# Kernel optimization log

Hardware: AMD Instinct MI355X
Metric: run time of the kernel (lower is better)

Reference implementation:

```python
import jax, jax.numpy as jnp
import numpy as np

B, N, K, C, D_IN, D_OUT = 64, 207, 32, 8, 64, 64


def setup_inputs() -> dict:
    key = jax.random.key(0)
    k1, k2, k3 = jax.random.split(key, 3)
    clustered_index_topk = jax.random.randint(k1, (B, N, K), 0, C)
    weightedDinput_topk = jax.random.normal(k2, (B, N, K, D_IN), dtype=jnp.float32)
    W = jax.random.normal(k3, (C, D_OUT, D_IN), dtype=jnp.float32) * 0.05
    return {"clustered_index_topk": clustered_index_topk,
            "weightedDinput_topk": weightedDinput_topk,
            "W": W}


def reference(clustered_index_topk, weightedDinput_topk, W):
    # one-hot over classes: [B, N, K, C]
    onehot = (clustered_index_topk[..., None] == jnp.arange(C)).astype(weightedDinput_topk.dtype)
    # per-class masked sum over top-k neighbors: [B, N, C, D_IN]
    sums = jnp.einsum('bnkc,bnkd->bncd', onehot, weightedDinput_topk)
    # per-class counts, clamped to >= 1 (matches torch.clamp(class_count, 1))
    counts = jnp.maximum(onehot.sum(axis=2), 1.0)  # [B, N, C]
    mean = sums / counts[..., None]
    # per-class Linear (weight [out, in], no bias) + Tanh -> [B, N, C, D_OUT]
    out = jnp.tanh(jnp.einsum('bncd,cod->bnco', mean, W))
    return out
```

## Files before the change

### kernel.cpp

```cpp
#include <hip/hip_runtime.h>
#include <cstddef>

#define BB 64
#define NN 207
#define KK 32
#define CC 8
#define DIN 64
#define DOUT 64
#define TILE 16
#define NT 13
#define MPADH 68

__device__ __forceinline__ float fast_tanh(float v) {
    float e = __expf(2.0f * v);
    return 1.0f - 2.0f * __builtin_amdgcn_rcpf(e + 1.0f);
}

__device__ __forceinline__ unsigned int f2bf(float f) {
    union { float f; unsigned int u; } v; v.f = f;
    return (v.u + 0x7fffu + ((v.u >> 16) & 1u)) >> 16;
}

__device__ __forceinline__ void fma16(float4& a, const float4 m,
                                      const float4 w0, const float4 w1,
                                      const float4 w2, const float4 w3) {
    a.x = fmaf(m.x, w0.x, a.x); a.y = fmaf(m.x, w0.y, a.y);
    a.z = fmaf(m.x, w0.z, a.z); a.w = fmaf(m.x, w0.w, a.w);
    a.x = fmaf(m.y, w1.x, a.x); a.y = fmaf(m.y, w1.y, a.y);
    a.z = fmaf(m.y, w1.z, a.z); a.w = fmaf(m.y, w1.w, a.w);
    a.x = fmaf(m.z, w2.x, a.x); a.y = fmaf(m.z, w2.y, a.y);
    a.z = fmaf(m.z, w2.z, a.z); a.w = fmaf(m.z, w2.w, a.w);
    a.x = fmaf(m.w, w3.x, a.x); a.y = fmaf(m.w, w3.y, a.y);
    a.z = fmaf(m.w, w3.z, a.z); a.w = fmaf(m.w, w3.w, a.w);
}

template<bool USE_WT>
__device__ __forceinline__ void load_w4(const float* __restrict__ Wtc,
                                        const float* __restrict__ Wc,
                                        int o0, int dc,
                                        float4& w0, float4& w1, float4& w2, float4& w3) {
    if (USE_WT) {
        w0 = *(const float4*)(Wtc + (size_t)(dc * 4 + 0) * DOUT);
        w1 = *(const float4*)(Wtc + (size_t)(dc * 4 + 1) * DOUT);
        w2 = *(const float4*)(Wtc + (size_t)(dc * 4 + 2) * DOUT);
        w3 = *(const float4*)(Wtc + (size_t)(dc * 4 + 3) * DOUT);
    } else {
        float4 a0 = *(const float4*)(Wc + (size_t)(o0 + 0) * DIN + dc * 4);
        float4 a1 = *(const float4*)(Wc + (size_t)(o0 + 1) * DIN + dc * 4);
        float4 a2 = *(const float4*)(Wc + (size_t)(o0 + 2) * DIN + dc * 4);
        float4 a3 = *(const float4*)(Wc + (size_t)(o0 + 3) * DIN + dc * 4);
        w0 = make_float4(a0.x, a1.x, a2.x, a3.x);
        w1 = make_float4(a0.y, a1.y, a2.y, a3.y);
        w2 = make_float4(a0.z, a1.z, a2.z, a3.z);
        w3 = make_float4(a0.w, a1.w, a2.w, a3.w);
    }
}

__global__ __launch_bounds__(256) void transpose_W_kernel(
    const float* __restrict__ W, float* __restrict__ Wt)
{
    __shared__ float t[DIN * (DOUT + 1)];
    const int c   = blockIdx.x;
    const int tid = threadIdx.x;
    const float* __restrict__ Wc  = W  + (size_t)c * DOUT * DIN;
    float* __restrict__       Wtc = Wt + (size_t)c * DIN * DOUT;
    #pragma unroll
    for (int r = 0; r < 16; ++r) {
        const int i = r * 256 + tid;
        const int o = i >> 6, d = i & 63;
        t[d * (DOUT + 1) + o] = Wc[i];
    }
    __syncthreads();
    #pragma unroll
    for (int r = 0; r < 16; ++r) {
        const int i = r * 256 + tid;
        const int d = i >> 6, o = i & 63;
        Wtc[i] = t[d * (DOUT + 1) + o];
    }
}

template<bool USE_WT>
__global__ __launch_bounds__(256, 6) void ordered_gcn_kernel(
    const int* __restrict__ idx,
    const float* __restrict__ x,
    const float* __restrict__ W,
    const float* __restrict__ Wt,
    float* __restrict__ out)
{
    __shared__ int            idx_s[TILE * KK];
    __shared__ float          inv_s[TILE * CC];
    __shared__ unsigned short mean_s[TILE * CC * MPADH];

    const int tid = threadIdx.x;
    const int b   = blockIdx.y;
    const int n0  = blockIdx.x * TILE;

    #pragma unroll
    for (int r = 0; r < 2; ++r) {
        const int i = r * 256 + tid;
        const int P = i >> 5, k = i & 31;
        int n = n0 + P; if (n > NN - 1) n = NN - 1;
        idx_s[i] = idx[((size_t)(b * NN + n)) * KK + k];
    }
    __syncthreads();

    if (tid < TILE * CC) {
        const int P = tid >> 3, c = tid & 7;
        int cnt = 0;
        #pragma unroll
        for (int k = 0; k < KK; ++k) cnt += (idx_s[P * KK + k] == c) ? 1 : 0;
        inv_s[tid] = 1.0f / (float)(cnt > 1 ? cnt : 1);
    }

    {
        const int p  = tid >> 4;
        const int d4 = (tid & 15) * 4;
        int n = n0 + p; if (n > NN - 1) n = NN - 1;
        const float* __restrict__ xp = x + ((size_t)(b * NN + n)) * KK * DIN + d4;

        float4 acc[CC];
        #pragma unroll
        for (int c = 0; c < CC; ++c) acc[c] = make_float4(0.f, 0.f, 0.f, 0.f);

        #pragma unroll 1
        for (int g = 0; g < 2; ++g) {
            float4 v[8];
            #pragma unroll
            for (int j = 0; j < 8; ++j)
                v[j] = *(const float4*)(xp + (size_t)(g * 8 + j) * DIN);
            #pragma unroll
            for (int j = 0; j < 8; ++j) {
                const int ca = idx_s[p * KK + g * 8 + j];
                #pragma unroll
                for (int c = 0; c < CC; ++c) {
                    const float mf = (ca == c) ? 1.0f : 0.0f;
                    acc[c].x = fmaf(mf, v[j].x, acc[c].x);
                    acc[c].y = fmaf(mf, v[j].y, acc[c].y);
                    acc[c].z = fmaf(mf, v[j].z, acc[c].z);
                    acc[c].w = fmaf(mf, v[j].w, acc[c].w);
                }
            }
        }
        #pragma unroll 1
        for (int g = 2; g < 4; ++g) {
            float4 v[8];
            #pragma unroll
            for (int j = 0; j < 8; ++j)
                v[j] = *(const float4*)(xp + (size_t)(g * 8 + j) * DIN);
            #pragma unroll
            for (int j = 0; j < 8; ++j) {
                const int ca = idx_s[p * KK + g * 8 + j];
                #pragma unroll
                for (int c = 0; c < CC; ++c) {
                    const float mf = (ca == c) ? 1.0f : 0.0f;
                    acc[c].x = fmaf(mf, v[j].x, acc[c].x);
                    acc[c].y = fmaf(mf, v[j].y, acc[c].y);
                    acc[c].z = fmaf(mf, v[j].z, acc[c].z);
                    acc[c].w = fmaf(mf, v[j].w, acc[c].w);
                }
            }
        }
        __syncthreads();

        #pragma unroll
        for (int c = 0; c < CC; ++c) {
            const float s = inv_s[p * CC + c];
            const unsigned int lo = f2bf(acc[c].x * s) | (f2bf(acc[c].y * s) << 16);
            const unsigned int hi = f2bf(acc[c].z * s) | (f2bf(acc[c].w * s) << 16);
            *(uint2*)(&mean_s[(p * CC + c) * MPADH + d4]) = make_uint2(lo, hi);
        }
    }
    __syncthreads();

    {
        const int ph = tid >> 7;
        const int c2 = (tid >> 4) & 7;
        const int o0 = (tid & 15) * 4;
        const float* __restrict__ Wtc = Wt + (size_t)c2 * DIN * DOUT + o0;
        const float* __restrict__ Wc  = W  + (size_t)c2 * DOUT * DIN;

        float4 acc2[8];
        #pragma unroll
        for (int pp = 0; pp < 8; ++pp) acc2[pp] = make_float4(0.f, 0.f, 0.f, 0.f);

        #pragma unroll 2
        for (int dc = 0; dc < 16; ++dc) {
            float4 w0, w1, w2, w3;
            load_w4<USE_WT>(Wtc, Wc, o0, dc, w0, w1, w2, w3);
            #pragma unroll
            for (int pp = 0; pp < 8; ++pp) {
                const uint2 mw = *(const uint2*)(&mean_s[((ph * 8 + pp) * CC + c2) * MPADH + dc * 4]);
                float4 m;
                m.x = __uint_as_float(mw.x << 16);
                m.y = __uint_as_float(mw.x & 0xffff0000u);
                m.z = __uint_as_float(mw.y << 16);
                m.w = __uint_as_float(mw.y & 0xffff0000u);
                fma16(acc2[pp], m, w0, w1, w2, w3);
            }
        }

        #pragma unroll
        for (int pp = 0; pp < 8; ++pp) {
            const int nn = n0 + ph * 8 + pp;
            if (nn < NN) {
                float4 r;
                r.x = fast_tanh(acc2[pp].x);
                r.y = fast_tanh(acc2[pp].y);
                r.z = fast_tanh(acc2[pp].z);
                r.w = fast_tanh(acc2[pp].w);
                *(float4*)(out + (((size_t)(b * NN + nn)) * CC + c2) * DOUT + o0) = r;
            }
        }
    }
}

extern "C" void kernel_launch(void* const* d_in, const int* in_sizes, int n_in,
                              void* d_out, int out_size, void* d_ws, size_t ws_size,
                              hipStream_t stream) {
    const int*   idx = (const int*)d_in[0];
    const float* x   = (const float*)d_in[1];
    const float* W   = (const float*)d_in[2];
    float* out = (float*)d_out;
    float* Wt  = (float*)d_ws;

    dim3 grid(NT, BB);
    dim3 block(256);
    const size_t wt_bytes = (size_t)CC * DIN * DOUT * sizeof(float);
    if (ws_size >= wt_bytes) {
        transpose_W_kernel<<<dim3(CC), block, 0, stream>>>(W, Wt);
        ordered_gcn_kernel<true><<<grid, block, 0, stream>>>(idx, x, W, Wt, out);
    } else {
        ordered_gcn_kernel<false><<<grid, block, 0, stream>>>(idx, x, W, Wt, out);
    }
}
```

Measured before the change: 205.4 us.

## Shrink node tile to 4 and split neighbor reduction across lanes with shuffles

Reduces the node tile from 16 to 4, which quadruples the grid to 52x64 blocks. Each wavefront now handles one node, with four lane groups each summing 8 of the 32 neighbors and combining the partial sums through xor shuffles. The bf16 packing of the mean in shared memory is replaced by fp32 storage, and launch bounds drop from 6 to 4 blocks per SIMD. The aim is more parallelism and less per-thread serial loading latency. The cost is that each weight load is reused across only 2 nodes instead of 8, raising W traffic through L1/L2, and the shuffles add instructions.

New measurement: 188.4 us. 8.3% less time.

```diff
diff --git a/kernel.cpp b/kernel.cpp
--- a/kernel.cpp
+++ b/kernel.cpp
@@ -7,18 +7,13 @@
 #define CC 8
 #define DIN 64
 #define DOUT 64
-#define TILE 16
-#define NT 13
-#define MPADH 68
+#define TILE 4
+#define NT 52
+#define MPAD 68
 
 __device__ __forceinline__ float fast_tanh(float v) {
     float e = __expf(2.0f * v);
     return 1.0f - 2.0f * __builtin_amdgcn_rcpf(e + 1.0f);
-}
-
-__device__ __forceinline__ unsigned int f2bf(float f) {
-    union { float f; unsigned int u; } v; v.f = f;
-    return (v.u + 0x7fffu + ((v.u >> 16) & 1u)) >> 16;
 }
 
 __device__ __forceinline__ void fma16(float4& a, const float4 m,
@@ -80,27 +75,25 @@
 }
 
 template<bool USE_WT>
-__global__ __launch_bounds__(256, 6) void ordered_gcn_kernel(
+__global__ __launch_bounds__(256, 4) void ordered_gcn_kernel(
     const int* __restrict__ idx,
     const float* __restrict__ x,
     const float* __restrict__ W,
     const float* __restrict__ Wt,
     float* __restrict__ out)
 {
-    __shared__ int            idx_s[TILE * KK];
-    __shared__ float          inv_s[TILE * CC];
-    __shared__ unsigned short mean_s[TILE * CC * MPADH];
+    __shared__ int   idx_s[TILE * KK];
+    __shared__ float inv_s[TILE * CC];
+    __shared__ float mean_s[TILE * CC * MPAD];
 
     const int tid = threadIdx.x;
     const int b   = blockIdx.y;
     const int n0  = blockIdx.x * TILE;
 
-    #pragma unroll
-    for (int r = 0; r < 2; ++r) {
-        const int i = r * 256 + tid;
-        const int P = i >> 5, k = i & 31;
+    if (tid < TILE * KK) {
+        const int P = tid >> 5, k = tid & 31;
         int n = n0 + P; if (n > NN - 1) n = NN - 1;
-        idx_s[i] = idx[((size_t)(b * NN + n)) * KK + k];
+        idx_s[tid] = idx[((size_t)(b * NN + n)) * KK + k];
     }
     __syncthreads();
 
@@ -113,103 +106,96 @@
     }
 
     {
-        const int p  = tid >> 4;
-        const int d4 = (tid & 15) * 4;
+        const int p  = tid >> 6;
+        const int ln = tid & 63;
+        const int kq = ln >> 4;
+        const int d4 = (ln & 15) * 4;
         int n = n0 + p; if (n > NN - 1) n = NN - 1;
-        const float* __restrict__ xp = x + ((size_t)(b * NN + n)) * KK * DIN + d4;
+        const float* __restrict__ xp =
+            x + (((size_t)(b * NN + n)) * KK + kq * 8) * DIN + d4;
+
+        float4 v[8];
+        #pragma unroll
+        for (int j = 0; j < 8; ++j)
+            v[j] = *(const float4*)(xp + (size_t)j * DIN);
 
         float4 acc[CC];
         #pragma unroll
         for (int c = 0; c < CC; ++c) acc[c] = make_float4(0.f, 0.f, 0.f, 0.f);
 
-        #pragma unroll 1
-        for (int g = 0; g < 2; ++g) {
-            float4 v[8];
+        #pragma unroll
+        for (int j = 0; j < 8; ++j) {
+            const int ca = idx_s[p * KK + kq * 8 + j];
             #pragma unroll
-            for (int j = 0; j < 8; ++j)
-                v[j] = *(const float4*)(xp + (size_t)(g * 8 + j) * DIN);
+            for (int c = 0; c < CC; ++c) {
+                const float mf = (ca == c) ? 1.0f : 0.0f;
+                acc[c].x = fmaf(mf, v[j].x, acc[c].x);
+                acc[c].y = fmaf(mf, v[j].y, acc[c].y);
+                acc[c].z = fmaf(mf, v[j].z, acc[c].z);
+                acc[c].w = fmaf(mf, v[j].w, acc[c].w);
+            }
+        }
+
+        #pragma unroll
+        for (int c = 0; c < CC; ++c) {
+            float* a = (float*)&acc[c];
             #pragma unroll
-            for (int j = 0; j < 8; ++j) {
-                const int ca = idx_s[p * KK + g * 8 + j];
-                #pragma unroll
-                for (int c = 0; c < CC; ++c) {
-                    const float mf = (ca == c) ? 1.0f : 0.0f;
-                    acc[c].x = fmaf(mf, v[j].x, acc[c].x);
-                    acc[c].y = fmaf(mf, v[j].y, acc[c].y);
-                    acc[c].z = fmaf(mf, v[j].z, acc[c].z);
-                    acc[c].w = fmaf(mf, v[j].w, acc[c].w);
-                }
+            for (int q = 0; q < 4; ++q) {
+                a[q] += __shfl_xor(a[q], 16, 64);
+                a[q] += __shfl_xor(a[q], 32, 64);
             }
         }
-        #pragma unroll 1
-        for (int g = 2; g < 4; ++g) {
-            float4 v[8];
+
+        __syncthreads();
+        if (kq == 0) {
             #pragma unroll
-            for (int j = 0; j < 8; ++j)
-                v[j] = *(const float4*)(xp + (size_t)(g * 8 + j) * DIN);
-            #pragma unroll
-            for (int j = 0; j < 8; ++j) {
-                const int ca = idx_s[p * KK + g * 8 + j];
-                #pragma unroll
-                for (int c = 0; c < CC; ++c) {
-                    const float mf = (ca == c) ? 1.0f : 0.0f;
-                    acc[c].x = fmaf(mf, v[j].x, acc[c].x);
-                    acc[c].y = fmaf(mf, v[j].y, acc[c].y);
-                    acc[c].z = fmaf(mf, v[j].z, acc[c].z);
-                    acc[c].w = fmaf(mf, v[j].w, acc[c].w);
-                }
+            for (int c = 0; c < CC; ++c) {
+                const float s = inv_s[p * CC + c];
+                float4 m;
+                m.x = acc[c].x * s; m.y = acc[c].y * s;
+                m.z = acc[c].z * s; m.w = acc[c].w * s;
+                *(float4*)(&mean_s[(p * CC + c) * MPAD + d4]) = m;
             }
         }
-        __syncthreads();
-
-        #pragma unroll
-        for (int c = 0; c < CC; ++c) {
-            const float s = inv_s[p * CC + c];
-            const unsigned int lo = f2bf(acc[c].x * s) | (f2bf(acc[c].y * s) << 16);
-            const unsigned int hi = f2bf(acc[c].z * s) | (f2bf(acc[c].w * s) << 16);
-            *(uint2*)(&mean_s[(p * CC + c) * MPADH + d4]) = make_uint2(lo, hi);
-        }
     }
     __syncthreads();
 
     {
-        const int ph = tid >> 7;
-        const int c2 = (tid >> 4) & 7;
-        const int o0 = (tid & 15) * 4;
+        const int c2 = tid >> 5;
+        const int l2 = tid & 31;
+        const int ph = l2 >> 4;
+        const int o0 = (l2 & 15) * 4;
+        const int p0 = ph * 2, p1 = ph * 2 + 1;
+
         const float* __restrict__ Wtc = Wt + (size_t)c2 * DIN * DOUT + o0;
         const float* __restrict__ Wc  = W  + (size_t)c2 * DOUT * DIN;
 
-        float4 acc2[8];
-        #pragma unroll
-        for (int pp = 0; pp < 8; ++pp) acc2[pp] = make_float4(0.f, 0.f, 0.f, 0.f);
+        float4 a0 = make_float4(0.f, 0.f, 0.f, 0.f);
+        float4 a1 = make_float4(0.f, 0.f, 0.f, 0.f);
 
         #pragma unroll 2
         for (int dc = 0; dc < 16; ++dc) {
             float4 w0, w1, w2, w3;
             load_w4<USE_WT>(Wtc, Wc, o0, dc, w0, w1, w2, w3);
-            #pragma unroll
-            for (int pp = 0; pp < 8; ++pp) {
-                const uint2 mw = *(const uint2*)(&mean_s[((ph * 8 + pp) * CC + c2) * MPADH + dc * 4]);
-                float4 m;
-                m.x = __uint_as_float(mw.x << 16);
-                m.y = __uint_as_float(mw.x & 0xffff0000u);
-                m.z = __uint_as_float(mw.y << 16);
-                m.w = __uint_as_float(mw.y & 0xffff0000u);
-                fma16(acc2[pp], m, w0, w1, w2, w3);
-            }
-        }
-
-        #pragma unroll
-        for (int pp = 0; pp < 8; ++pp) {
-            const int nn = n0 + ph * 8 + pp;
-            if (nn < NN) {
-                float4 r;
-                r.x = fast_tanh(acc2[pp].x);
-                r.y = fast_tanh(acc2[pp].y);
-                r.z = fast_tanh(acc2[pp].z);
-                r.w = fast_tanh(acc2[pp].w);
-                *(float4*)(out + (((size_t)(b * NN + nn)) * CC + c2) * DOUT + o0) = r;
-            }
+            const float4 m0 = *(const float4*)(&mean_s[(p0 * CC + c2) * MPAD + dc * 4]);
+            const float4 m1 = *(const float4*)(&mean_s[(p1 * CC + c2) * MPAD + dc * 4]);
+            fma16(a0, m0, w0, w1, w2, w3);
+            fma16(a1, m1, w0, w1, w2, w3);
+        }
+
+        const int nn0 = n0 + p0;
+        if (nn0 < NN) {
+            float4 r;
+            r.x = fast_tanh(a0.x); r.y = fast_tanh(a0.y);
+            r.z = fast_tanh(a0.z); r.w = fast_tanh(a0.w);
+            *(float4*)(out + (((size_t)(b * NN + nn0)) * CC + c2) * DOUT + o0) = r;
+        }
+        const int nn1 = n0 + p1;
+        if (nn1 < NN) {
+            float4 r;
+            r.x = fast_tanh(a1.x); r.y = fast_tanh(a1.y);
+            r.z = fast_tanh(a1.z); r.w = fast_tanh(a1.w);
+            *(float4*)(out + (((size_t)(b * NN + nn1)) * CC + c2) * DOUT + o0) = r;
         }
     }
 }
```
